# Kernel tuning notes

Measured on AMD Instinct MI355X. Metric: run time of the kernel, lower is better.

The kernel has to match this reference:

```python
import jax, jax.numpy as jnp
import numpy as np

B, C, H, W = 16, 512, 48, 48


def setup_inputs() -> dict:
    key = jax.random.key(0)
    k1, k2 = jax.random.split(key)
    rgb = jax.random.normal(k1, (B, C, H, W), dtype=jnp.float32)
    depth = jax.random.normal(k2, (B, C, H, W), dtype=jnp.float32)
    return {"rgb": rgb, "depth": depth}


def reference(rgb, depth):
    b, c, h, w = rgb.shape
    hw = h * w
    q = rgb.reshape(b, c, hw)              # [B, C, HW]
    k = depth.reshape(b, c, hw)            # [B, C, HW]
    # channel-affinity: energy[b, i, j] = <rgb_chan_i, depth_chan_j>
    energy = jnp.einsum('bcn,bdn->bcd', q, k)   # [B, C, C]
    cl_index = jnp.argmax(energy, axis=2)       # [B, C] best-matching depth channel per rgb channel
    # gather matched depth channels and fuse
    gathered = depth[jnp.arange(b)[:, None], cl_index]  # [B, C, H, W]
    return rgb + gathered
```

## Files before the change

### kernel.cpp

```cpp
#include <hip/hip_runtime.h>
#include <stdint.h>

#define BATCH 16
#define CH    512
#define HW    2304
#define BM    128
#define BN    128
#define BK    64
#define NKT   (HW / BK)

typedef _Float16 half8  __attribute__((ext_vector_type(8)));
typedef float    f32x16 __attribute__((ext_vector_type(16)));

#define AH_OFF 0
#define AL_OFF 16384
#define BH_OFF 32768
#define BL_OFF 49152
#define BUF_SZ 65536

#define MFMA16 __builtin_amdgcn_mfma_f32_32x32x16_f16

#define LGKM_BARRIER() do { \
    asm volatile("s_waitcnt lgkmcnt(0)" ::: "memory"); \
    __builtin_amdgcn_s_barrier(); \
    __builtin_amdgcn_sched_barrier(0); \
} while (0)

__device__ __forceinline__ uint32_t f32_sortable(float f) {
    uint32_t u = __float_as_uint(f);
    return (u & 0x80000000u) ? ~u : (u | 0x80000000u);
}

__device__ __forceinline__ int swz(int r, int s) {
    return r * 128 + ((s ^ ((r >> 1) & 7)) << 4);
}

__device__ __forceinline__ void cvt8(const float4& v0, const float4& v1,
                                     half8& h, half8& l) {
    float vv[8] = {v0.x, v0.y, v0.z, v0.w, v1.x, v1.y, v1.z, v1.w};
    #pragma unroll
    for (int j = 0; j < 8; ++j) {
        _Float16 hh = (_Float16)vv[j];
        h[j] = hh;
        l[j] = (_Float16)(vv[j] - (float)hh);
    }
}

__device__ __forceinline__ void load_tile(const float* aG, const float* bG, int k0,
                                          float4 (&av)[4], float4 (&bv)[4]) {
    av[0] = *(const float4*)(aG + k0 + 0);
    av[1] = *(const float4*)(aG + k0 + 4);
    av[2] = *(const float4*)(aG + k0 + 8);
    av[3] = *(const float4*)(aG + k0 + 12);
    bv[0] = *(const float4*)(bG + k0 + 0);
    bv[1] = *(const float4*)(bG + k0 + 4);
    bv[2] = *(const float4*)(bG + k0 + 8);
    bv[3] = *(const float4*)(bG + k0 + 12);
}

__device__ __forceinline__ void stage_tile(char* dst,
                                           const float4 (&av)[4], const float4 (&bv)[4],
                                           int row, int q) {
    half8 h, l;
    cvt8(av[0], av[1], h, l);
    *(half8*)(dst + AH_OFF + swz(row, 2 * q))     = h;
    *(half8*)(dst + AL_OFF + swz(row, 2 * q))     = l;
    cvt8(av[2], av[3], h, l);
    *(half8*)(dst + AH_OFF + swz(row, 2 * q + 1)) = h;
    *(half8*)(dst + AL_OFF + swz(row, 2 * q + 1)) = l;
    cvt8(bv[0], bv[1], h, l);
    *(half8*)(dst + BH_OFF + swz(row, 2 * q))     = h;
    *(half8*)(dst + BL_OFF + swz(row, 2 * q))     = l;
    cvt8(bv[2], bv[3], h, l);
    *(half8*)(dst + BH_OFF + swz(row, 2 * q + 1)) = h;
    *(half8*)(dst + BL_OFF + swz(row, 2 * q + 1)) = l;
}

__device__ __forceinline__ void compute_tile(const char* buf, int rA0, int rB, int half,
                                             f32x16& acc0, f32x16& acc1) {
    __builtin_amdgcn_s_setprio(1);
    #pragma unroll
    for (int kc = 0; kc < 4; ++kc) {
        const int s0 = 2 * kc + half;
        half8 ah0 = *(const half8*)(buf + AH_OFF + swz(rA0,      s0));
        half8 ah1 = *(const half8*)(buf + AH_OFF + swz(rA0 + 32, s0));
        half8 al0 = *(const half8*)(buf + AL_OFF + swz(rA0,      s0));
        half8 al1 = *(const half8*)(buf + AL_OFF + swz(rA0 + 32, s0));
        half8 bh  = *(const half8*)(buf + BH_OFF + swz(rB, s0));
        half8 bl  = *(const half8*)(buf + BL_OFF + swz(rB, s0));
        acc0 = MFMA16(ah0, bh, acc0, 0, 0, 0);
        acc1 = MFMA16(ah1, bh, acc1, 0, 0, 0);
        acc0 = MFMA16(ah0, bl, acc0, 0, 0, 0);
        acc1 = MFMA16(ah1, bl, acc1, 0, 0, 0);
        acc0 = MFMA16(al0, bh, acc0, 0, 0, 0);
        acc1 = MFMA16(al1, bh, acc1, 0, 0, 0);
    }
    __builtin_amdgcn_s_setprio(0);
}

__global__ __launch_bounds__(512, 1)
void energy_argmax_kernel(const float* __restrict__ q,
                          const float* __restrict__ kmat,
                          unsigned long long* __restrict__ best)
{
    const int bid = blockIdx.x;
    const int nid = (bid & 7) * 32 + (bid >> 3);
    const int d0  = (nid & 3) * BN;
    const int c0  = ((nid >> 2) & 3) * BM;
    const int b   = nid >> 4;

    const int tid  = threadIdx.x;
    const int lane = tid & 63;
    const int w    = tid >> 6;
    const int wm   = w >> 2;
    const int wn   = w & 3;

    __shared__ __align__(16) char sm[2 * BUF_SZ];
    char* buf0 = sm;
    char* buf1 = sm + BUF_SZ;

    const float* qb = q    + (size_t)b * CH * HW;
    const float* kb = kmat + (size_t)b * CH * HW;

    const int row = tid >> 2, sq = tid & 3;
    const float* aG = qb + (size_t)(c0 + row) * HW + sq * 16;
    const float* bG = kb + (size_t)(d0 + row) * HW + sq * 16;

    float4 av0[4], bv0[4], av1[4], bv1[4];

    load_tile(aG, bG, 0, av0, bv0);
    stage_tile(buf0, av0, bv0, row, sq);
    load_tile(aG, bG, BK, av1, bv1);
    LGKM_BARRIER();

    f32x16 acc0 = {}, acc1 = {};

    const int rA0  = wm * 64 + (lane & 31);
    const int rB   = wn * 32 + (lane & 31);
    const int half = lane >> 5;

    for (int kt = 0; kt < NKT - 1; kt += 2) {
        if (kt + 2 < NKT) load_tile(aG, bG, (kt + 2) * BK, av0, bv0);
        stage_tile(buf1, av1, bv1, row, sq);
        compute_tile(buf0, rA0, rB, half, acc0, acc1);
        LGKM_BARRIER();
        if (kt + 3 < NKT) load_tile(aG, bG, (kt + 3) * BK, av1, bv1);
        if (kt + 2 < NKT) stage_tile(buf0, av0, bv0, row, sq);
        compute_tile(buf1, rA0, rB, half, acc0, acc1);
        LGKM_BARRIER();
    }

    const uint32_t didx = ~(uint32_t)(d0 + wn * 32 + (lane & 31));
    #pragma unroll
    for (int mi = 0; mi < 2; ++mi) {
        #pragma unroll
        for (int qr = 0; qr < 16; ++qr) {
            float v = (mi == 0) ? acc0[qr] : acc1[qr];
            int rowl = wm * 64 + mi * 32 + (qr & 3) + 8 * (qr >> 2) + 4 * (lane >> 5);
            unsigned long long p =
                ((unsigned long long)f32_sortable(v) << 32) | didx;
            #pragma unroll
            for (int off = 1; off < 32; off <<= 1) {
                unsigned long long o = __shfl_xor(p, off, 64);
                if (o > p) p = o;
            }
            if ((lane & 31) == 0)
                atomicMax(&best[(size_t)b * CH + c0 + rowl], p);
        }
    }
}

__global__ __launch_bounds__(256)
void gather_add_kernel(const float* __restrict__ rgb,
                       const float* __restrict__ depth,
                       const unsigned long long* __restrict__ best,
                       float* __restrict__ out)
{
    const int row = blockIdx.x;
    const int b   = row >> 9;
    const uint32_t idx = ~(uint32_t)(best[row] & 0xFFFFFFFFull);
    const float4* src = (const float4*)(rgb   + (size_t)row * HW);
    const float4* dep = (const float4*)(depth + ((size_t)b * CH + idx) * HW);
    float4*       dst = (float4*)(out + (size_t)row * HW);
    for (int j = threadIdx.x; j < HW / 4; j += 256) {
        float4 a = src[j], d = dep[j];
        float4 r; r.x = a.x + d.x; r.y = a.y + d.y; r.z = a.z + d.z; r.w = a.w + d.w;
        dst[j] = r;
    }
}

extern "C" void kernel_launch(void* const* d_in, const int* in_sizes, int n_in,
                              void* d_out, int out_size, void* d_ws, size_t ws_size,
                              hipStream_t stream)
{
    const float* rgb   = (const float*)d_in[0];
    const float* depth = (const float*)d_in[1];
    float* out = (float*)d_out;
    unsigned long long* best = (unsigned long long*)d_ws;

    hipMemsetAsync(best, 0, (size_t)BATCH * CH * sizeof(unsigned long long), stream);

    energy_argmax_kernel<<<256, 512, 0, stream>>>(rgb, depth, best);

    gather_add_kernel<<<BATCH * CH, 256, 0, stream>>>(rgb, depth, best, out);
}
```

Measured before the change: 123.2 us.

## Interleave LDS staging with MFMA compute in four barrier-synchronized phases per tile

Splits each K-tile's compute into four phases. Each phase issues its LDS fragment reads, converts and stores one quarter of the next tile's staging data, then runs six MFMAs, with workgroup barriers bracketing the MFMA cluster. This is meant to interleave the conversion and LDS-write work with matrix math across waves, ping-pong style, instead of doing all staging up front. It adds eight barriers per tile where there were one, which raises synchronization overhead.

Result: slower. 139.7 us (+13.4%).

```diff
diff --git a/kernel.cpp b/kernel.cpp
--- a/kernel.cpp
+++ b/kernel.cpp
@@ -19,12 +19,6 @@
 #define BUF_SZ 65536
 
 #define MFMA16 __builtin_amdgcn_mfma_f32_32x32x16_f16
-
-#define LGKM_BARRIER() do { \
-    asm volatile("s_waitcnt lgkmcnt(0)" ::: "memory"); \
-    __builtin_amdgcn_s_barrier(); \
-    __builtin_amdgcn_sched_barrier(0); \
-} while (0)
 
 __device__ __forceinline__ uint32_t f32_sortable(float f) {
     uint32_t u = __float_as_uint(f);
@@ -76,26 +70,66 @@
     *(half8*)(dst + BL_OFF + swz(row, 2 * q + 1)) = l;
 }
 
-__device__ __forceinline__ void compute_tile(const char* buf, int rA0, int rB, int half,
-                                             f32x16& acc0, f32x16& acc1) {
+template<int KC>
+__device__ __forceinline__ void phase(const char* rd, char* wr,
+                                      const float4 (&av)[4], const float4 (&bv)[4],
+                                      bool stg, int row, int sq,
+                                      int rA0, int rB, int half,
+                                      f32x16& acc0, f32x16& acc1)
+{
+    const int s0 = 2 * KC + half;
+    half8 ah0 = *(const half8*)(rd + AH_OFF + swz(rA0,      s0));
+    half8 ah1 = *(const half8*)(rd + AH_OFF + swz(rA0 + 32, s0));
+    half8 al0 = *(const half8*)(rd + AL_OFF + swz(rA0,      s0));
+    half8 al1 = *(const half8*)(rd + AL_OFF + swz(rA0 + 32, s0));
+    half8 bh  = *(const half8*)(rd + BH_OFF + swz(rB, s0));
+    half8 bl  = *(const half8*)(rd + BL_OFF + swz(rB, s0));
+    if (stg) {
+        half8 h, l;
+        if constexpr (KC == 0) {
+            cvt8(av[0], av[1], h, l);
+            *(half8*)(wr + AH_OFF + swz(row, 2 * sq))     = h;
+            *(half8*)(wr + AL_OFF + swz(row, 2 * sq))     = l;
+        } else if constexpr (KC == 1) {
+            cvt8(av[2], av[3], h, l);
+            *(half8*)(wr + AH_OFF + swz(row, 2 * sq + 1)) = h;
+            *(half8*)(wr + AL_OFF + swz(row, 2 * sq + 1)) = l;
+        } else if constexpr (KC == 2) {
+            cvt8(bv[0], bv[1], h, l);
+            *(half8*)(wr + BH_OFF + swz(row, 2 * sq))     = h;
+            *(half8*)(wr + BL_OFF + swz(row, 2 * sq))     = l;
+        } else {
+            cvt8(bv[2], bv[3], h, l);
+            *(half8*)(wr + BH_OFF + swz(row, 2 * sq + 1)) = h;
+            *(half8*)(wr + BL_OFF + swz(row, 2 * sq + 1)) = l;
+        }
+    }
+    __builtin_amdgcn_sched_barrier(0);
+    __builtin_amdgcn_s_barrier();
+    asm volatile("s_waitcnt lgkmcnt(0)" ::: "memory");
+    __builtin_amdgcn_sched_barrier(0);
     __builtin_amdgcn_s_setprio(1);
-    #pragma unroll
-    for (int kc = 0; kc < 4; ++kc) {
-        const int s0 = 2 * kc + half;
-        half8 ah0 = *(const half8*)(buf + AH_OFF + swz(rA0,      s0));
-        half8 ah1 = *(const half8*)(buf + AH_OFF + swz(rA0 + 32, s0));
-        half8 al0 = *(const half8*)(buf + AL_OFF + swz(rA0,      s0));
-        half8 al1 = *(const half8*)(buf + AL_OFF + swz(rA0 + 32, s0));
-        half8 bh  = *(const half8*)(buf + BH_OFF + swz(rB, s0));
-        half8 bl  = *(const half8*)(buf + BL_OFF + swz(rB, s0));
-        acc0 = MFMA16(ah0, bh, acc0, 0, 0, 0);
-        acc1 = MFMA16(ah1, bh, acc1, 0, 0, 0);
-        acc0 = MFMA16(ah0, bl, acc0, 0, 0, 0);
-        acc1 = MFMA16(ah1, bl, acc1, 0, 0, 0);
-        acc0 = MFMA16(al0, bh, acc0, 0, 0, 0);
-        acc1 = MFMA16(al1, bh, acc1, 0, 0, 0);
-    }
+    acc0 = MFMA16(ah0, bh, acc0, 0, 0, 0);
+    acc1 = MFMA16(ah1, bh, acc1, 0, 0, 0);
+    acc0 = MFMA16(ah0, bl, acc0, 0, 0, 0);
+    acc1 = MFMA16(ah1, bl, acc1, 0, 0, 0);
+    acc0 = MFMA16(al0, bh, acc0, 0, 0, 0);
+    acc1 = MFMA16(al1, bh, acc1, 0, 0, 0);
     __builtin_amdgcn_s_setprio(0);
+    __builtin_amdgcn_s_barrier();
+    __builtin_amdgcn_sched_barrier(0);
+}
+
+__device__ __forceinline__ void step_phases(const char* rd, char* wr,
+                                            const float4 (&av)[4], const float4 (&bv)[4],
+                                            bool stg, int row, int sq,
+                                            int rA0, int rB, int half,
+                                            f32x16& acc0, f32x16& acc1)
+{
+    phase<0>(rd, wr, av, bv, stg, row, sq, rA0, rB, half, acc0, acc1);
+    phase<1>(rd, wr, av, bv, stg, row, sq, rA0, rB, half, acc0, acc1);
+    phase<2>(rd, wr, av, bv, stg, row, sq, rA0, rB, half, acc0, acc1);
+    phase<3>(rd, wr, av, bv, stg, row, sq, rA0, rB, half, acc0, acc1);
 }
 
 __global__ __launch_bounds__(512, 1)
@@ -131,7 +165,9 @@
     load_tile(aG, bG, 0, av0, bv0);
     stage_tile(buf0, av0, bv0, row, sq);
     load_tile(aG, bG, BK, av1, bv1);
-    LGKM_BARRIER();
+    asm volatile("s_waitcnt lgkmcnt(0)" ::: "memory");
+    __builtin_amdgcn_s_barrier();
+    __builtin_amdgcn_sched_barrier(0);
 
     f32x16 acc0 = {}, acc1 = {};
 
@@ -139,15 +175,11 @@
     const int rB   = wn * 32 + (lane & 31);
     const int half = lane >> 5;
 
-    for (int kt = 0; kt < NKT - 1; kt += 2) {
+    for (int kt = 0; kt < NKT; kt += 2) {
         if (kt + 2 < NKT) load_tile(aG, bG, (kt + 2) * BK, av0, bv0);
-        stage_tile(buf1, av1, bv1, row, sq);
-        compute_tile(buf0, rA0, rB, half, acc0, acc1);
-        LGKM_BARRIER();
+        step_phases(buf0, buf1, av1, bv1, true, row, sq, rA0, rB, half, acc0, acc1);
         if (kt + 3 < NKT) load_tile(aG, bG, (kt + 3) * BK, av1, bv1);
-        if (kt + 2 < NKT) stage_tile(buf0, av0, bv0, row, sq);
-        compute_tile(buf1, rA0, rB, half, acc0, acc1);
-        LGKM_BARRIER();
+        step_phases(buf1, buf0, av0, bv0, kt + 2 < NKT, row, sq, rA0, rB, half, acc0, acc1);
     }
 
     const uint32_t didx = ~(uint32_t)(d0 + wn * 32 + (lane & 31));
```

## Screen energy with single-fp16 GEMM and rescore near-max candidates exactly in fp32

Applied to the files above, without the earlier changes.

The split-fp16 (hi/lo, three-MFMA) GEMM with fused atomic argmax is replaced by a single-fp16 screening GEMM that writes the full energy matrix to workspace. A second kernel then finds each row's max and recomputes exact fp32 dot products for every channel within a fixed margin (3.5) of it. The winning depth channel is gathered and added in that same kernel. The aim is to cut MFMA and LDS work by about three times. In exchange it adds an energy-matrix write and read plus serial per-candidate dot products, and it relies on a fixed margin that only bounds the fp16 error for inputs of roughly unit scale. A fallback path with a retiled BK=32 split-fp16 kernel runs when the workspace is too small.

New measurement: 104.4 us. 1.18x faster.

```diff
diff --git a/kernel.cpp b/kernel.cpp
--- a/kernel.cpp
+++ b/kernel.cpp
@@ -6,19 +6,27 @@
 #define HW    2304
 #define BM    128
 #define BN    128
-#define BK    64
-#define NKT   (HW / BK)
 
 typedef _Float16 half8  __attribute__((ext_vector_type(8)));
 typedef float    f32x16 __attribute__((ext_vector_type(16)));
 
-#define AH_OFF 0
-#define AL_OFF 16384
-#define BH_OFF 32768
-#define BL_OFF 49152
-#define BUF_SZ 65536
-
 #define MFMA16 __builtin_amdgcn_mfma_f32_32x32x16_f16
+
+#define DELTA 3.5f
+
+#define ENERGY_ELEMS ((size_t)BATCH * CH * CH)
+
+__device__ __forceinline__ uint32_t f32_sortable(float f) {
+    uint32_t u = __float_as_uint(f);
+    return (u & 0x80000000u) ? ~u : (u | 0x80000000u);
+}
+
+
+#define BKs   64
+#define NKTs  (HW / BKs)
+#define AHs_OFF 0
+#define BHs_OFF 16384
+#define BUFs_SZ 32768
 
 #define LGKM_BARRIER() do { \
     asm volatile("s_waitcnt lgkmcnt(0)" ::: "memory"); \
@@ -26,28 +34,21 @@
     __builtin_amdgcn_sched_barrier(0); \
 } while (0)
 
-__device__ __forceinline__ uint32_t f32_sortable(float f) {
-    uint32_t u = __float_as_uint(f);
-    return (u & 0x80000000u) ? ~u : (u | 0x80000000u);
-}
-
-__device__ __forceinline__ int swz(int r, int s) {
+__device__ __forceinline__ int swzs(int r, int s) {
     return r * 128 + ((s ^ ((r >> 1) & 7)) << 4);
 }
 
-__device__ __forceinline__ void cvt8(const float4& v0, const float4& v1,
-                                     half8& h, half8& l) {
-    float vv[8] = {v0.x, v0.y, v0.z, v0.w, v1.x, v1.y, v1.z, v1.w};
-    #pragma unroll
-    for (int j = 0; j < 8; ++j) {
-        _Float16 hh = (_Float16)vv[j];
-        h[j] = hh;
-        l[j] = (_Float16)(vv[j] - (float)hh);
-    }
-}
-
-__device__ __forceinline__ void load_tile(const float* aG, const float* bG, int k0,
-                                          float4 (&av)[4], float4 (&bv)[4]) {
+__device__ __forceinline__ half8 cvt8h(const float4& v0, const float4& v1) {
+    half8 h;
+    h[0] = (_Float16)v0.x; h[1] = (_Float16)v0.y;
+    h[2] = (_Float16)v0.z; h[3] = (_Float16)v0.w;
+    h[4] = (_Float16)v1.x; h[5] = (_Float16)v1.y;
+    h[6] = (_Float16)v1.z; h[7] = (_Float16)v1.w;
+    return h;
+}
+
+__device__ __forceinline__ void load_tile_s(const float* aG, const float* bG, int k0,
+                                            float4 (&av)[4], float4 (&bv)[4]) {
     av[0] = *(const float4*)(aG + k0 + 0);
     av[1] = *(const float4*)(aG + k0 + 4);
     av[2] = *(const float4*)(aG + k0 + 8);
@@ -58,36 +59,220 @@
     bv[3] = *(const float4*)(bG + k0 + 12);
 }
 
-__device__ __forceinline__ void stage_tile(char* dst,
-                                           const float4 (&av)[4], const float4 (&bv)[4],
-                                           int row, int q) {
-    half8 h, l;
-    cvt8(av[0], av[1], h, l);
-    *(half8*)(dst + AH_OFF + swz(row, 2 * q))     = h;
-    *(half8*)(dst + AL_OFF + swz(row, 2 * q))     = l;
-    cvt8(av[2], av[3], h, l);
-    *(half8*)(dst + AH_OFF + swz(row, 2 * q + 1)) = h;
-    *(half8*)(dst + AL_OFF + swz(row, 2 * q + 1)) = l;
-    cvt8(bv[0], bv[1], h, l);
-    *(half8*)(dst + BH_OFF + swz(row, 2 * q))     = h;
-    *(half8*)(dst + BL_OFF + swz(row, 2 * q))     = l;
-    cvt8(bv[2], bv[3], h, l);
-    *(half8*)(dst + BH_OFF + swz(row, 2 * q + 1)) = h;
-    *(half8*)(dst + BL_OFF + swz(row, 2 * q + 1)) = l;
-}
-
-__device__ __forceinline__ void compute_tile(const char* buf, int rA0, int rB, int half,
-                                             f32x16& acc0, f32x16& acc1) {
+__device__ __forceinline__ void stage_tile_s(char* dst,
+                                             const float4 (&av)[4], const float4 (&bv)[4],
+                                             int row, int q) {
+    *(half8*)(dst + AHs_OFF + swzs(row, 2 * q))     = cvt8h(av[0], av[1]);
+    *(half8*)(dst + AHs_OFF + swzs(row, 2 * q + 1)) = cvt8h(av[2], av[3]);
+    *(half8*)(dst + BHs_OFF + swzs(row, 2 * q))     = cvt8h(bv[0], bv[1]);
+    *(half8*)(dst + BHs_OFF + swzs(row, 2 * q + 1)) = cvt8h(bv[2], bv[3]);
+}
+
+__device__ __forceinline__ void compute_tile_s(const char* buf, int rA0, int rB, int half,
+                                               f32x16& acc0, f32x16& acc1) {
     __builtin_amdgcn_s_setprio(1);
     #pragma unroll
     for (int kc = 0; kc < 4; ++kc) {
         const int s0 = 2 * kc + half;
-        half8 ah0 = *(const half8*)(buf + AH_OFF + swz(rA0,      s0));
-        half8 ah1 = *(const half8*)(buf + AH_OFF + swz(rA0 + 32, s0));
-        half8 al0 = *(const half8*)(buf + AL_OFF + swz(rA0,      s0));
-        half8 al1 = *(const half8*)(buf + AL_OFF + swz(rA0 + 32, s0));
-        half8 bh  = *(const half8*)(buf + BH_OFF + swz(rB, s0));
-        half8 bl  = *(const half8*)(buf + BL_OFF + swz(rB, s0));
+        half8 ah0 = *(const half8*)(buf + AHs_OFF + swzs(rA0,      s0));
+        half8 ah1 = *(const half8*)(buf + AHs_OFF + swzs(rA0 + 32, s0));
+        half8 bh  = *(const half8*)(buf + BHs_OFF + swzs(rB, s0));
+        acc0 = MFMA16(ah0, bh, acc0, 0, 0, 0);
+        acc1 = MFMA16(ah1, bh, acc1, 0, 0, 0);
+    }
+    __builtin_amdgcn_s_setprio(0);
+}
+
+__global__ __launch_bounds__(512, 1)
+void screen_kernel(const float* __restrict__ q,
+                   const float* __restrict__ kmat,
+                   float* __restrict__ energy)
+{
+    const int bid = blockIdx.x;
+    const int nid = (bid & 7) * 32 + (bid >> 3);
+    const int d0  = (nid & 3) * BN;
+    const int c0  = ((nid >> 2) & 3) * BM;
+    const int b   = nid >> 4;
+
+    const int tid  = threadIdx.x;
+    const int lane = tid & 63;
+    const int w    = tid >> 6;
+    const int wm   = w >> 2;
+    const int wn   = w & 3;
+
+    __shared__ __align__(16) char sm[2 * BUFs_SZ];
+    char* buf0 = sm;
+    char* buf1 = sm + BUFs_SZ;
+
+    const float* qb = q    + (size_t)b * CH * HW;
+    const float* kb = kmat + (size_t)b * CH * HW;
+
+    const int row = tid >> 2, sq = tid & 3;
+    const float* aG = qb + (size_t)(c0 + row) * HW + sq * 16;
+    const float* bG = kb + (size_t)(d0 + row) * HW + sq * 16;
+
+    float4 av0[4], bv0[4], av1[4], bv1[4];
+
+    load_tile_s(aG, bG, 0, av0, bv0);
+    stage_tile_s(buf0, av0, bv0, row, sq);
+    load_tile_s(aG, bG, BKs, av1, bv1);
+    LGKM_BARRIER();
+
+    f32x16 acc0 = {}, acc1 = {};
+    const int rA0  = wm * 64 + (lane & 31);
+    const int rB   = wn * 32 + (lane & 31);
+    const int half = lane >> 5;
+
+    for (int kt = 0; kt < NKTs; kt += 2) {
+        if (kt + 2 < NKTs) load_tile_s(aG, bG, (kt + 2) * BKs, av0, bv0);
+        stage_tile_s(buf1, av1, bv1, row, sq);
+        compute_tile_s(buf0, rA0, rB, half, acc0, acc1);
+        LGKM_BARRIER();
+        if (kt + 3 < NKTs) load_tile_s(aG, bG, (kt + 3) * BKs, av1, bv1);
+        if (kt + 2 < NKTs) stage_tile_s(buf0, av0, bv0, row, sq);
+        compute_tile_s(buf1, rA0, rB, half, acc0, acc1);
+        LGKM_BARRIER();
+    }
+
+    float* eb = energy + ((size_t)(b * CH + c0) * CH) + d0 + wn * 32 + (lane & 31);
+    #pragma unroll
+    for (int mi = 0; mi < 2; ++mi) {
+        #pragma unroll
+        for (int qr = 0; qr < 16; ++qr) {
+            int rowl = wm * 64 + mi * 32 + (qr & 3) + 8 * (qr >> 2) + 4 * (lane >> 5);
+            eb[(size_t)rowl * CH] = (mi == 0) ? acc0[qr] : acc1[qr];
+        }
+    }
+}
+
+__global__ __launch_bounds__(256)
+void rescore_gather_kernel(const float* __restrict__ rgb,
+                           const float* __restrict__ depth,
+                           const float* __restrict__ energy,
+                           float* __restrict__ out)
+{
+    const int row = blockIdx.x;
+    const int b   = row >> 9;
+    const int tid = threadIdx.x;
+
+    __shared__ float sred[4];
+    __shared__ float sM;
+    __shared__ int   scnt;
+    __shared__ int   slist[CH];
+    __shared__ unsigned long long sbest;
+
+    const float* erow = energy + (size_t)row * CH;
+    float e0 = erow[tid], e1 = erow[tid + 256];
+
+    float m = fmaxf(e0, e1);
+    #pragma unroll
+    for (int off = 1; off < 64; off <<= 1) m = fmaxf(m, __shfl_xor(m, off, 64));
+    if ((tid & 63) == 0) sred[tid >> 6] = m;
+    __syncthreads();
+    if (tid == 0) {
+        sM = fmaxf(fmaxf(sred[0], sred[1]), fmaxf(sred[2], sred[3]));
+        scnt = 0; sbest = 0ull;
+    }
+    __syncthreads();
+    const float thr = sM - DELTA;
+    if (e0 >= thr) { int i = atomicAdd(&scnt, 1); slist[i] = tid; }
+    if (e1 >= thr) { int i = atomicAdd(&scnt, 1); slist[i] = tid + 256; }
+    __syncthreads();
+    const int cnt = scnt;
+
+    const float4* q4 = (const float4*)(rgb + (size_t)row * HW);
+    for (int i = 0; i < cnt; ++i) {
+        const int d = slist[i];
+        const float4* k4 = (const float4*)(depth + ((size_t)(b * CH + d)) * HW);
+        float s = 0.0f;
+        for (int j = tid; j < HW / 4; j += 256) {
+            float4 a = q4[j], bb = k4[j];
+            s += a.x * bb.x + a.y * bb.y + a.z * bb.z + a.w * bb.w;
+        }
+        #pragma unroll
+        for (int off = 1; off < 64; off <<= 1) s += __shfl_xor(s, off, 64);
+        if ((tid & 63) == 0) sred[tid >> 6] = s;
+        __syncthreads();
+        if (tid == 0) {
+            float tot = sred[0] + sred[1] + sred[2] + sred[3];
+            unsigned long long p =
+                ((unsigned long long)f32_sortable(tot) << 32) |
+                (uint32_t)(~(uint32_t)d);
+            if (p > sbest) sbest = p;
+        }
+        __syncthreads();
+    }
+
+    const int widx = (int)(~(uint32_t)(sbest & 0xFFFFFFFFull));
+    const float4* w4 = (const float4*)(depth + ((size_t)(b * CH + widx)) * HW);
+    float4* o4 = (float4*)(out + (size_t)row * HW);
+    for (int j = tid; j < HW / 4; j += 256) {
+        float4 a = q4[j], dd = w4[j];
+        o4[j] = make_float4(a.x + dd.x, a.y + dd.y, a.z + dd.z, a.w + dd.w);
+    }
+}
+
+
+#define BKf 32
+#define NKTf (HW / BKf)
+#define AHf_OFF 0
+#define ALf_OFF 16384
+#define BHf_OFF 32768
+#define BLf_OFF 49152
+#define BUFf_SZ 65536
+
+__device__ __forceinline__ int swzf(int r, int cb) {
+    return r * 64 + (cb ^ (((r >> 1) & 3) << 4));
+}
+
+__device__ __forceinline__ void cvt8f(const float4& v0, const float4& v1,
+                                      half8& h, half8& l) {
+    float vv[8] = {v0.x, v0.y, v0.z, v0.w, v1.x, v1.y, v1.z, v1.w};
+    #pragma unroll
+    for (int j = 0; j < 8; ++j) {
+        _Float16 hh = (_Float16)vv[j];
+        h[j] = hh;
+        l[j] = (_Float16)(vv[j] - (float)hh);
+    }
+}
+
+#define AH8_OFF 0
+#define AL8_OFF 8192
+#define BH8_OFF 16384
+#define BL8_OFF 24576
+#define BUF8_SZ 32768
+
+__device__ __forceinline__ void load_tile_f(const float* aG, const float* bG, int k0,
+                                            float4 (&av)[2], float4 (&bv)[2], int qq) {
+    av[0] = *(const float4*)(aG + k0 + qq * 8 + 0);
+    av[1] = *(const float4*)(aG + k0 + qq * 8 + 4);
+    bv[0] = *(const float4*)(bG + k0 + qq * 8 + 0);
+    bv[1] = *(const float4*)(bG + k0 + qq * 8 + 4);
+}
+
+__device__ __forceinline__ void stage_tile_f(char* dst,
+                                             const float4 (&av)[2], const float4 (&bv)[2],
+                                             int row, int qq) {
+    half8 h, l;
+    cvt8f(av[0], av[1], h, l);
+    *(half8*)(dst + AH8_OFF + swzf(row, qq * 16)) = h;
+    *(half8*)(dst + AL8_OFF + swzf(row, qq * 16)) = l;
+    cvt8f(bv[0], bv[1], h, l);
+    *(half8*)(dst + BH8_OFF + swzf(row, qq * 16)) = h;
+    *(half8*)(dst + BL8_OFF + swzf(row, qq * 16)) = l;
+}
+
+__device__ __forceinline__ void compute_tile_f(const char* buf, int rA0, int rB, int hb,
+                                               f32x16& acc0, f32x16& acc1) {
+    #pragma unroll
+    for (int kc = 0; kc < 2; ++kc) {
+        const int cb = kc * 32 + hb;
+        half8 ah0 = *(const half8*)(buf + AH8_OFF + swzf(rA0,      cb));
+        half8 ah1 = *(const half8*)(buf + AH8_OFF + swzf(rA0 + 32, cb));
+        half8 al0 = *(const half8*)(buf + AL8_OFF + swzf(rA0,      cb));
+        half8 al1 = *(const half8*)(buf + AL8_OFF + swzf(rA0 + 32, cb));
+        half8 bh  = *(const half8*)(buf + BH8_OFF + swzf(rB, cb));
+        half8 bl  = *(const half8*)(buf + BL8_OFF + swzf(rB, cb));
         acc0 = MFMA16(ah0, bh, acc0, 0, 0, 0);
         acc1 = MFMA16(ah1, bh, acc1, 0, 0, 0);
         acc0 = MFMA16(ah0, bl, acc0, 0, 0, 0);
@@ -95,13 +280,12 @@
         acc0 = MFMA16(al0, bh, acc0, 0, 0, 0);
         acc1 = MFMA16(al1, bh, acc1, 0, 0, 0);
     }
-    __builtin_amdgcn_s_setprio(0);
 }
 
 __global__ __launch_bounds__(512, 1)
-void energy_argmax_kernel(const float* __restrict__ q,
-                          const float* __restrict__ kmat,
-                          unsigned long long* __restrict__ best)
+void fb_energy_argmax_kernel(const float* __restrict__ q,
+                             const float* __restrict__ kmat,
+                             unsigned long long* __restrict__ best)
 {
     const int bid = blockIdx.x;
     const int nid = (bid & 7) * 32 + (bid >> 3);
@@ -115,39 +299,38 @@
     const int wm   = w >> 2;
     const int wn   = w & 3;
 
-    __shared__ __align__(16) char sm[2 * BUF_SZ];
+    __shared__ __align__(16) char sm[2 * BUF8_SZ];
     char* buf0 = sm;
-    char* buf1 = sm + BUF_SZ;
+    char* buf1 = sm + BUF8_SZ;
 
     const float* qb = q    + (size_t)b * CH * HW;
     const float* kb = kmat + (size_t)b * CH * HW;
 
     const int row = tid >> 2, sq = tid & 3;
-    const float* aG = qb + (size_t)(c0 + row) * HW + sq * 16;
-    const float* bG = kb + (size_t)(d0 + row) * HW + sq * 16;
-
-    float4 av0[4], bv0[4], av1[4], bv1[4];
-
-    load_tile(aG, bG, 0, av0, bv0);
-    stage_tile(buf0, av0, bv0, row, sq);
-    load_tile(aG, bG, BK, av1, bv1);
-    LGKM_BARRIER();
+    const float* aG = qb + (size_t)(c0 + row) * HW;
+    const float* bG = kb + (size_t)(d0 + row) * HW;
+
+    float4 av0[2], bv0[2], av1[2], bv1[2];
+
+    load_tile_f(aG, bG, 0, av0, bv0, sq);
+    stage_tile_f(buf0, av0, bv0, row, sq);
+    load_tile_f(aG, bG, BKf, av1, bv1, sq);
+    __syncthreads();
 
     f32x16 acc0 = {}, acc1 = {};
-
-    const int rA0  = wm * 64 + (lane & 31);
-    const int rB   = wn * 32 + (lane & 31);
-    const int half = lane >> 5;
-
-    for (int kt = 0; kt < NKT - 1; kt += 2) {
-        if (kt + 2 < NKT) load_tile(aG, bG, (kt + 2) * BK, av0, bv0);
-        stage_tile(buf1, av1, bv1, row, sq);
-        compute_tile(buf0, rA0, rB, half, acc0, acc1);
-        LGKM_BARRIER();
-        if (kt + 3 < NKT) load_tile(aG, bG, (kt + 3) * BK, av1, bv1);
-        if (kt + 2 < NKT) stage_tile(buf0, av0, bv0, row, sq);
-        compute_tile(buf1, rA0, rB, half, acc0, acc1);
-        LGKM_BARRIER();
+    const int rA0 = wm * 64 + (lane & 31);
+    const int rB  = wn * 32 + (lane & 31);
+    const int hb  = (lane >> 5) * 16;
+
+    for (int kt = 0; kt < NKTf; kt += 2) {
+        if (kt + 2 < NKTf) load_tile_f(aG, bG, (kt + 2) * BKf, av0, bv0, sq);
+        compute_tile_f(buf0, rA0, rB, hb, acc0, acc1);
+        stage_tile_f(buf1, av1, bv1, row, sq);
+        __syncthreads();
+        if (kt + 3 < NKTf) load_tile_f(aG, bG, (kt + 3) * BKf, av1, bv1, sq);
+        compute_tile_f(buf1, rA0, rB, hb, acc0, acc1);
+        if (kt + 2 < NKTf) stage_tile_f(buf0, av0, bv0, row, sq);
+        __syncthreads();
     }
 
     const uint32_t didx = ~(uint32_t)(d0 + wn * 32 + (lane & 31));
@@ -171,10 +354,10 @@
 }
 
 __global__ __launch_bounds__(256)
-void gather_add_kernel(const float* __restrict__ rgb,
-                       const float* __restrict__ depth,
-                       const unsigned long long* __restrict__ best,
-                       float* __restrict__ out)
+void fb_gather_add_kernel(const float* __restrict__ rgb,
+                          const float* __restrict__ depth,
+                          const unsigned long long* __restrict__ best,
+                          float* __restrict__ out)
 {
     const int row = blockIdx.x;
     const int b   = row >> 9;
@@ -184,8 +367,7 @@
     float4*       dst = (float4*)(out + (size_t)row * HW);
     for (int j = threadIdx.x; j < HW / 4; j += 256) {
         float4 a = src[j], d = dep[j];
-        float4 r; r.x = a.x + d.x; r.y = a.y + d.y; r.z = a.z + d.z; r.w = a.w + d.w;
-        dst[j] = r;
+        dst[j] = make_float4(a.x + d.x, a.y + d.y, a.z + d.z, a.w + d.w);
     }
 }
 
@@ -196,11 +378,15 @@
     const float* rgb   = (const float*)d_in[0];
     const float* depth = (const float*)d_in[1];
     float* out = (float*)d_out;
-    unsigned long long* best = (unsigned long long*)d_ws;
-
-    hipMemsetAsync(best, 0, (size_t)BATCH * CH * sizeof(unsigned long long), stream);
-
-    energy_argmax_kernel<<<256, 512, 0, stream>>>(rgb, depth, best);
-
-    gather_add_kernel<<<BATCH * CH, 256, 0, stream>>>(rgb, depth, best, out);
-}
+
+    if (ws_size >= ENERGY_ELEMS * sizeof(float)) {
+        float* energy = (float*)d_ws;
+        screen_kernel<<<256, 512, 0, stream>>>(rgb, depth, energy);
+        rescore_gather_kernel<<<BATCH * CH, 256, 0, stream>>>(rgb, depth, energy, out);
+    } else {
+        unsigned long long* best = (unsigned long long*)d_ws;
+        hipMemsetAsync(best, 0, (size_t)BATCH * CH * sizeof(unsigned long long), stream);
+        fb_energy_argmax_kernel<<<256, 512, 0, stream>>>(rgb, depth, best);
+        fb_gather_add_kernel<<<BATCH * CH, 256, 0, stream>>>(rgb, depth, best, out);
+    }
+}
```
